# Optimization experiments

Measured on AMD Instinct MI355X. Metric: run time of the kernel, lower is better.

## Reference

```python
import jax, jax.numpy as jnp
import numpy as np

B, C, L = 8, 512, 2048
CK = C // 8  # key/query dim of SAGAN attention


def setup_inputs() -> dict:
    key = jax.random.key(0)
    ks = jax.random.split(key, 4)
    s = 0.02  # init scale for weights
    x = jax.random.normal(ks[0], (B, C, L), dtype=jnp.float32)
    Wf = jax.random.normal(ks[1], (CK, C), dtype=jnp.float32) * s
    Wg = jax.random.normal(ks[2], (CK, C), dtype=jnp.float32) * s
    Wh = jax.random.normal(ks[3], (C, C), dtype=jnp.float32) * s
    bf = jnp.zeros((CK,), dtype=jnp.float32)
    bg = jnp.zeros((CK,), dtype=jnp.float32)
    bh = jnp.zeros((C,), dtype=jnp.float32)
    return {"x": x, "Wf": Wf, "bf": bf, "Wg": Wg, "bg": bg, "Wh": Wh, "bh": bh}


def reference(x, Wf, bf, Wg, bg, Wh, bh):
    # conv1x1 projections == channel-mixing matmuls
    f = jnp.einsum('kc,bcl->bkl', Wf, x) + bf[None, :, None]   # (B, CK, L)
    g = jnp.einsum('kc,bcl->bkl', Wg, x) + bg[None, :, None]   # (B, CK, L)
    h = jnp.einsum('oc,bcl->bol', Wh, x) + bh[None, :, None]   # (B, C, L)
    # att[b, i, j] = sum_k f[b,k,i] * g[b,k,j]  (NOTE: no 1/sqrt(d) scale, as in source)
    att = jnp.einsum('bki,bkj->bij', f, g)                      # (B, L, L)
    att = jax.nn.softmax(att, axis=-1)
    self_att = jnp.einsum('bcj,bij->bci', h, att)               # (B, C, L)
    return self_att + x
```

## Files before the change

### kernel.cpp

```cpp
#include <hip/hip_runtime.h>
#include <math.h>
#include <stdint.h>

#define BATCH 8
#define CH    512
#define SEQ   2048
#define CKDIM 64

typedef __attribute__((ext_vector_type(8))) short bf16x8;
typedef __attribute__((ext_vector_type(4))) float f32x4;

__device__ __forceinline__ unsigned short f2b(float f) {
    union { float f; uint32_t u; } v; v.f = f;
    uint32_t u = v.u;
    u += 0x7fffu + ((u >> 16) & 1u);
    return (unsigned short)(u >> 16);
}
__device__ __forceinline__ float b2f(unsigned short h) {
    union { uint32_t u; float f; } v; v.u = ((uint32_t)h) << 16;
    return v.f;
}

__global__ __launch_bounds__(256) void transpose_cast_kernel(
    const float* __restrict__ x, unsigned short* __restrict__ xt)
{
    __shared__ float t[64][65];
    const int b = blockIdx.z, l0 = blockIdx.x * 64, c0 = blockIdx.y * 64;
    const int tx = threadIdx.x & 63, ty = threadIdx.x >> 6;
    #pragma unroll
    for (int q = 0; q < 16; ++q)
        t[ty + q * 4][tx] = x[((size_t)b * CH + c0 + ty + q * 4) * SEQ + l0 + tx];
    __syncthreads();
    #pragma unroll
    for (int q = 0; q < 16; ++q)
        xt[((size_t)b * SEQ + l0 + ty + q * 4) * CH + c0 + tx] = f2b(t[tx][ty + q * 4]);
}

__global__ __launch_bounds__(256) void castw_kernel(
    const float* __restrict__ Wf, const float* __restrict__ Wg,
    const float* __restrict__ Wh, const float* __restrict__ bf_,
    const float* __restrict__ bg_, unsigned short* __restrict__ Wfgb,
    unsigned short* __restrict__ Whb, float* __restrict__ bias_fg)
{
    const int i = blockIdx.x * 256 + threadIdx.x;
    if (i < 128) bias_fg[i] = (i < 64) ? bf_[i] : bg_[i - 64];
    if (i < 65536) Wfgb[i] = f2b((i < 32768) ? Wf[i] : Wg[i - 32768]);
    if (i < 262144) Whb[i] = f2b(Wh[i]);
}

__device__ __attribute__((always_inline)) inline void gemm_core_nt(
    const unsigned short* __restrict__ A, const int ldA,
    const unsigned short* __restrict__ B, const int ldB,
    const int K,
    unsigned short* __restrict__ ldsA, unsigned short* __restrict__ ldsB,
    f32x4 acc[4][4])
{
    const int tid  = threadIdx.x;
    const int lane = tid & 63;
    const int wm   = tid >> 7;
    const int wn   = (tid >> 6) & 1;
    const int fr   = lane & 15;
    const int hi   = lane >> 4;
    const int xo   = lane & 7;

    int goA[4], goB[4], lo[4];
    #pragma unroll
    for (int it = 0; it < 4; ++it) {
        const int idx = tid + it * 256;
        const int row = idx >> 3;
        const int ch  = idx & 7;
        goA[it] = row * ldA + ch * 8;
        goB[it] = row * ldB + ch * 8;
        lo[it]  = row * 64 + ((ch ^ (row & 7)) * 8);
    }
    int aoff[4], boff[4];
    #pragma unroll
    for (int f = 0; f < 4; ++f) {
        aoff[f] = (wm * 64 + f * 16 + fr) * 64;
        boff[f] = (wn * 64 + f * 16 + fr) * 64;
    }
    const int coff0 = ((0 + hi) ^ xo) * 8;
    const int coff1 = ((4 + hi) ^ xo) * 8;

    uint4 ra[4], rb[4];
    #pragma unroll
    for (int it = 0; it < 4; ++it) {
        ra[it] = *(const uint4*)(A + goA[it]);
        rb[it] = *(const uint4*)(B + goB[it]);
    }

    for (int k0 = 0; k0 < K; k0 += 64) {
        #pragma unroll
        for (int it = 0; it < 4; ++it) {
            *(uint4*)&ldsA[lo[it]] = ra[it];
            *(uint4*)&ldsB[lo[it]] = rb[it];
        }
        __syncthreads();
        if (k0 + 64 < K) {
            #pragma unroll
            for (int it = 0; it < 4; ++it) {
                ra[it] = *(const uint4*)(A + goA[it] + k0 + 64);
                rb[it] = *(const uint4*)(B + goB[it] + k0 + 64);
            }
        }
        #pragma unroll
        for (int kk = 0; kk < 2; ++kk) {
            const int co = kk ? coff1 : coff0;
            bf16x8 af[4], bg[4];
            #pragma unroll
            for (int f = 0; f < 4; ++f) {
                af[f] = *(const bf16x8*)&ldsA[aoff[f] + co];
                bg[f] = *(const bf16x8*)&ldsB[boff[f] + co];
            }
            #pragma unroll
            for (int m = 0; m < 4; ++m)
                #pragma unroll
                for (int n = 0; n < 4; ++n)
                    acc[m][n] = __builtin_amdgcn_mfma_f32_16x16x32_bf16(
                        af[m], bg[n], acc[m][n], 0, 0, 0);
        }
        __syncthreads();
    }
}

__device__ __attribute__((always_inline)) inline void epilogue_store_bf16(
    unsigned short* __restrict__ lds, f32x4 acc[4][4],
    unsigned short* __restrict__ outBase, const int ldOut,
    const float* __restrict__ rowBias, const float* __restrict__ colBias)
{
    const int tid = threadIdx.x;
    const int lane = tid & 63;
    const int wm = tid >> 7, wn = (tid >> 6) & 1;
    const int fr = lane & 15, hi = lane >> 4;
    #pragma unroll
    for (int m = 0; m < 4; ++m) {
        const int m0 = wm * 64 + m * 16 + hi * 4;
        #pragma unroll
        for (int n = 0; n < 4; ++n) {
            const int nn = wn * 64 + n * 16 + fr;
            const float cb = colBias ? colBias[nn] : 0.f;
            #pragma unroll
            for (int e = 0; e < 4; ++e) {
                float v = acc[m][n][e] + cb;
                if (rowBias) v += rowBias[m0 + e];
                lds[(m0 + e) * 128 + nn] = f2b(v);
            }
        }
    }
    __syncthreads();
    #pragma unroll
    for (int q = 0; q < 8; ++q) {
        const int idx = tid + q * 256;
        const int row = idx >> 4, ch = idx & 15;
        *(uint4*)&outBase[(size_t)row * ldOut + ch * 8] =
            *(const uint4*)&lds[row * 128 + ch * 8];
    }
}

__global__ __launch_bounds__(256) void proj_fg_kernel(
    const unsigned short* __restrict__ xt, const unsigned short* __restrict__ Wfg,
    const float* __restrict__ bias_fg, unsigned short* __restrict__ fg_t)
{
    __shared__ unsigned short lds[16384];
    const int b = blockIdx.z, i0 = blockIdx.x * 128;
    const unsigned short* A = xt + ((size_t)b * SEQ + i0) * CH;
    f32x4 acc[4][4];
    const f32x4 z = {0.f, 0.f, 0.f, 0.f};
    #pragma unroll
    for (int m = 0; m < 4; ++m)
        #pragma unroll
        for (int n = 0; n < 4; ++n) acc[m][n] = z;
    gemm_core_nt(A, CH, Wfg, CH, CH, lds, lds + 8192, acc);
    epilogue_store_bf16(lds, acc, fg_t + ((size_t)b * SEQ + i0) * 128, 128,
                        nullptr, bias_fg);
}

__global__ __launch_bounds__(256) void proj_h_kernel(
    const unsigned short* __restrict__ xt, const unsigned short* __restrict__ Whb,
    const float* __restrict__ bh, unsigned short* __restrict__ h_b)
{
    __shared__ unsigned short lds[16384];
    const int b = blockIdx.z, l0 = blockIdx.x * 128, c0 = blockIdx.y * 128;
    const unsigned short* A = Whb + (size_t)c0 * CH;
    const unsigned short* B = xt + ((size_t)b * SEQ + l0) * CH;
    f32x4 acc[4][4];
    const f32x4 z = {0.f, 0.f, 0.f, 0.f};
    #pragma unroll
    for (int m = 0; m < 4; ++m)
        #pragma unroll
        for (int n = 0; n < 4; ++n) acc[m][n] = z;
    gemm_core_nt(A, CH, B, CH, CH, lds, lds + 8192, acc);
    epilogue_store_bf16(lds, acc,
                        h_b + ((size_t)b * CH + c0) * SEQ + l0, SEQ,
                        bh + c0, nullptr);
}

__global__ __launch_bounds__(256) void scores_kernel(
    const unsigned short* __restrict__ fg_t, unsigned short* __restrict__ att,
    int b0, long long attStride)
{
    __shared__ unsigned short lds[16384];
    const int b = b0 + blockIdx.z;
    const int j0 = blockIdx.x * 128, i0 = blockIdx.y * 128;
    const unsigned short* A = fg_t + ((size_t)b * SEQ + i0) * 128;
    const unsigned short* B = fg_t + ((size_t)b * SEQ + j0) * 128 + 64;
    f32x4 acc[4][4];
    const f32x4 z = {0.f, 0.f, 0.f, 0.f};
    #pragma unroll
    for (int m = 0; m < 4; ++m)
        #pragma unroll
        for (int n = 0; n < 4; ++n) acc[m][n] = z;
    gemm_core_nt(A, 128, B, 128, CKDIM, lds, lds + 8192, acc);
    unsigned short* outBase = att + (size_t)blockIdx.z * attStride +
                              (size_t)i0 * SEQ + j0;
    epilogue_store_bf16(lds, acc, outBase, SEQ, nullptr, nullptr);
}

__global__ __launch_bounds__(256) void softmax_kernel(
    unsigned short* __restrict__ att, long long attStride)
{
    const int w = threadIdx.x >> 6, lane = threadIdx.x & 63;
    uint4* rp = (uint4*)(att + (size_t)blockIdx.z * attStride +
                         ((size_t)blockIdx.x * 4 + w) * SEQ);
    uint4 v[4];
    float f[32];
    #pragma unroll
    for (int q = 0; q < 4; ++q) v[q] = rp[lane + q * 64];
    #pragma unroll
    for (int q = 0; q < 4; ++q) {
        const uint32_t w0 = v[q].x, w1 = v[q].y, w2 = v[q].z, w3 = v[q].w;
        f[q * 8 + 0] = b2f((unsigned short)(w0 & 0xffff));
        f[q * 8 + 1] = b2f((unsigned short)(w0 >> 16));
        f[q * 8 + 2] = b2f((unsigned short)(w1 & 0xffff));
        f[q * 8 + 3] = b2f((unsigned short)(w1 >> 16));
        f[q * 8 + 4] = b2f((unsigned short)(w2 & 0xffff));
        f[q * 8 + 5] = b2f((unsigned short)(w2 >> 16));
        f[q * 8 + 6] = b2f((unsigned short)(w3 & 0xffff));
        f[q * 8 + 7] = b2f((unsigned short)(w3 >> 16));
    }
    float mx = -INFINITY;
    #pragma unroll
    for (int q = 0; q < 32; ++q) mx = fmaxf(mx, f[q]);
    #pragma unroll
    for (int off = 32; off > 0; off >>= 1)
        mx = fmaxf(mx, __shfl_xor(mx, off));
    float s = 0.f;
    #pragma unroll
    for (int q = 0; q < 32; ++q) { f[q] = __expf(f[q] - mx); s += f[q]; }
    #pragma unroll
    for (int off = 32; off > 0; off >>= 1)
        s += __shfl_xor(s, off);
    const float inv = 1.f / s;
    #pragma unroll
    for (int q = 0; q < 4; ++q) {
        uint4 o;
        o.x = (uint32_t)f2b(f[q * 8 + 0] * inv) | ((uint32_t)f2b(f[q * 8 + 1] * inv) << 16);
        o.y = (uint32_t)f2b(f[q * 8 + 2] * inv) | ((uint32_t)f2b(f[q * 8 + 3] * inv) << 16);
        o.z = (uint32_t)f2b(f[q * 8 + 4] * inv) | ((uint32_t)f2b(f[q * 8 + 5] * inv) << 16);
        o.w = (uint32_t)f2b(f[q * 8 + 6] * inv) | ((uint32_t)f2b(f[q * 8 + 7] * inv) << 16);
        rp[lane + q * 64] = o;
    }
}

__global__ __launch_bounds__(256) void pv_kernel(
    const unsigned short* __restrict__ h_b, const unsigned short* __restrict__ att,
    const float* __restrict__ x, float* __restrict__ out,
    int b0, long long attStride)
{
    __shared__ unsigned short lds[16384];
    const int b = b0 + blockIdx.z;
    const int i0 = blockIdx.x * 128, c0 = blockIdx.y * 128;
    const unsigned short* A = h_b + ((size_t)b * CH + c0) * SEQ;
    const unsigned short* B = att + (size_t)blockIdx.z * attStride + (size_t)i0 * SEQ;
    f32x4 acc[4][4];
    const f32x4 z = {0.f, 0.f, 0.f, 0.f};
    #pragma unroll
    for (int m = 0; m < 4; ++m)
        #pragma unroll
        for (int n = 0; n < 4; ++n) acc[m][n] = z;
    gemm_core_nt(A, SEQ, B, SEQ, SEQ, lds, lds + 8192, acc);

    const int lane = threadIdx.x & 63;
    const int wm = threadIdx.x >> 7, wn = (threadIdx.x >> 6) & 1;
    const int fr = lane & 15, hi = lane >> 4;
    #pragma unroll
    for (int m = 0; m < 4; ++m)
        #pragma unroll
        for (int n = 0; n < 4; ++n) {
            const int i = i0 + wn * 64 + n * 16 + fr;
            #pragma unroll
            for (int e = 0; e < 4; ++e) {
                const int c = c0 + wm * 64 + m * 16 + hi * 4 + e;
                const size_t o = ((size_t)b * CH + c) * SEQ + i;
                out[o] = acc[m][n][e] + x[o];
            }
        }
}

extern "C" void kernel_launch(void* const* d_in, const int* in_sizes, int n_in,
                              void* d_out, int out_size, void* d_ws, size_t ws_size,
                              hipStream_t stream)
{
    const float* x  = (const float*)d_in[0];
    const float* Wf = (const float*)d_in[1];
    const float* bf_ = (const float*)d_in[2];
    const float* Wg = (const float*)d_in[3];
    const float* bg_ = (const float*)d_in[4];
    const float* Wh = (const float*)d_in[5];
    const float* bh = (const float*)d_in[6];
    float* out = (float*)d_out;

    unsigned short* ws = (unsigned short*)d_ws;
    size_t off = 0;
    unsigned short* xt   = ws + off; off += (size_t)BATCH * SEQ * CH;
    unsigned short* Wfgb = ws + off; off += 128 * CH;
    unsigned short* Whb  = ws + off; off += CH * CH;
    unsigned short* fg_t = ws + off; off += (size_t)BATCH * SEQ * 128;
    unsigned short* h_b  = ws + off; off += (size_t)BATCH * CH * SEQ;
    float* bias_fg = (float*)(ws + off); off += 256;
    unsigned short* att  = ws + off;

    const size_t need_multi = (off + (size_t)BATCH * SEQ * SEQ) * sizeof(unsigned short);
    const bool multi = ws_size >= need_multi;

    transpose_cast_kernel<<<dim3(SEQ / 64, CH / 64, BATCH), 256, 0, stream>>>(x, xt);
    castw_kernel<<<dim3(1024), 256, 0, stream>>>(Wf, Wg, Wh, bf_, bg_, Wfgb, Whb, bias_fg);
    proj_fg_kernel<<<dim3(SEQ / 128, 1, BATCH), 256, 0, stream>>>(xt, Wfgb, bias_fg, fg_t);
    proj_h_kernel<<<dim3(SEQ / 128, CH / 128, BATCH), 256, 0, stream>>>(xt, Whb, bh, h_b);

    if (multi) {
        const long long s = (long long)SEQ * SEQ;
        scores_kernel<<<dim3(SEQ / 128, SEQ / 128, BATCH), 256, 0, stream>>>(fg_t, att, 0, s);
        softmax_kernel<<<dim3(SEQ / 4, 1, BATCH), 256, 0, stream>>>(att, s);
        pv_kernel<<<dim3(SEQ / 128, CH / 128, BATCH), 256, 0, stream>>>(h_b, att, x, out, 0, s);
    } else {
        for (int b = 0; b < BATCH; ++b) {
            scores_kernel<<<dim3(SEQ / 128, SEQ / 128, 1), 256, 0, stream>>>(fg_t, att, b, 0);
            softmax_kernel<<<dim3(SEQ / 4, 1, 1), 256, 0, stream>>>(att, 0);
            pv_kernel<<<dim3(SEQ / 128, CH / 128, 1), 256, 0, stream>>>(h_b, att, x, out, b, 0);
        }
    }
}
```

Measured before the change: 370.3 us.

## Fuse scores, softmax and PV into a single flash-attention kernel

Replaces the separate scores, softmax and PV kernels, which write and re-read a full B×L×L bf16 attention matrix, with one online-softmax flash kernel. Each block handles 64 query rows and all 512 channels, streaming 64-key tiles of g and h with register prefetch and keeping S, P and h in LDS. This removes the large attention-matrix traffic and two launches. In exchange it launches only 256 blocks of 512 threads with about 90KB of LDS each, so occupancy and parallelism are low, and every j-tile goes through several barriers.

New measurement: 443.2 us. 19.7% more time.

```diff
diff --git a/kernel.cpp b/kernel.cpp
--- a/kernel.cpp
+++ b/kernel.cpp
@@ -15,10 +15,6 @@
     uint32_t u = v.u;
     u += 0x7fffu + ((u >> 16) & 1u);
     return (unsigned short)(u >> 16);
-}
-__device__ __forceinline__ float b2f(unsigned short h) {
-    union { uint32_t u; float f; } v; v.u = ((uint32_t)h) << 16;
-    return v.f;
 }
 
 __global__ __launch_bounds__(256) void transpose_cast_kernel(
@@ -195,119 +191,192 @@
                         bh + c0, nullptr);
 }
 
-__global__ __launch_bounds__(256) void scores_kernel(
-    const unsigned short* __restrict__ fg_t, unsigned short* __restrict__ att,
-    int b0, long long attStride)
-{
-    __shared__ unsigned short lds[16384];
-    const int b = b0 + blockIdx.z;
-    const int j0 = blockIdx.x * 128, i0 = blockIdx.y * 128;
-    const unsigned short* A = fg_t + ((size_t)b * SEQ + i0) * 128;
-    const unsigned short* B = fg_t + ((size_t)b * SEQ + j0) * 128 + 64;
+__global__ __launch_bounds__(512) void flash_kernel(
+    const unsigned short* __restrict__ fg_t,
+    const unsigned short* __restrict__ h_b,
+    const float* __restrict__ x,
+    float* __restrict__ out)
+{
+    __shared__ __align__(16) char smem[92160];
+    unsigned short* h_lds = (unsigned short*)smem;
+    unsigned short* P_lds = (unsigned short*)(smem + 65536);
+    float* S_lds = (float*)(smem + 73728);
+    float* m_lds = (float*)(smem + 91136);
+    float* l_lds = (float*)(smem + 91392);
+    float* a_lds = (float*)(smem + 91648);
+    float* trans = (float*)smem;
+
+    const int tid  = threadIdx.x;
+    const int w    = tid >> 6, lane = tid & 63;
+    const int fr   = lane & 15, hi = lane >> 4;
+    const int flat = blockIdx.x;
+    const int b    = flat & 7;
+    const int i0   = (flat >> 3) * 64;
+    const int ihalf = w & 1, jq = w >> 1;
+
+    if (tid < 64) { m_lds[tid] = -INFINITY; l_lds[tid] = 0.f; }
+
+    bf16x8 qf[2][2];
+    #pragma unroll
+    for (int m = 0; m < 2; ++m)
+        #pragma unroll
+        for (int kk = 0; kk < 2; ++kk)
+            qf[m][kk] = *(const bf16x8*)(fg_t +
+                ((size_t)b * SEQ + i0 + ihalf * 32 + m * 16 + fr) * 128 +
+                kk * 32 + hi * 8);
+
+    bf16x8 greg[2];
+    uint4 hreg[8];
+    #pragma unroll
+    for (int kk = 0; kk < 2; ++kk)
+        greg[kk] = *(const bf16x8*)(fg_t +
+            ((size_t)b * SEQ + jq * 16 + fr) * 128 + 64 + kk * 32 + hi * 8);
+    #pragma unroll
+    for (int q = 0; q < 8; ++q) {
+        const int id = tid + q * 512, c = id >> 3, ch = id & 7;
+        hreg[q] = *(const uint4*)(h_b + ((size_t)b * CH + c) * SEQ + ch * 8);
+    }
+
     f32x4 acc[4][4];
     const f32x4 z = {0.f, 0.f, 0.f, 0.f};
     #pragma unroll
     for (int m = 0; m < 4; ++m)
         #pragma unroll
         for (int n = 0; n < 4; ++n) acc[m][n] = z;
-    gemm_core_nt(A, 128, B, 128, CKDIM, lds, lds + 8192, acc);
-    unsigned short* outBase = att + (size_t)blockIdx.z * attStride +
-                              (size_t)i0 * SEQ + j0;
-    epilogue_store_bf16(lds, acc, outBase, SEQ, nullptr, nullptr);
-}
-
-__global__ __launch_bounds__(256) void softmax_kernel(
-    unsigned short* __restrict__ att, long long attStride)
-{
-    const int w = threadIdx.x >> 6, lane = threadIdx.x & 63;
-    uint4* rp = (uint4*)(att + (size_t)blockIdx.z * attStride +
-                         ((size_t)blockIdx.x * 4 + w) * SEQ);
-    uint4 v[4];
-    float f[32];
-    #pragma unroll
-    for (int q = 0; q < 4; ++q) v[q] = rp[lane + q * 64];
-    #pragma unroll
-    for (int q = 0; q < 4; ++q) {
-        const uint32_t w0 = v[q].x, w1 = v[q].y, w2 = v[q].z, w3 = v[q].w;
-        f[q * 8 + 0] = b2f((unsigned short)(w0 & 0xffff));
-        f[q * 8 + 1] = b2f((unsigned short)(w0 >> 16));
-        f[q * 8 + 2] = b2f((unsigned short)(w1 & 0xffff));
-        f[q * 8 + 3] = b2f((unsigned short)(w1 >> 16));
-        f[q * 8 + 4] = b2f((unsigned short)(w2 & 0xffff));
-        f[q * 8 + 5] = b2f((unsigned short)(w2 >> 16));
-        f[q * 8 + 6] = b2f((unsigned short)(w3 & 0xffff));
-        f[q * 8 + 7] = b2f((unsigned short)(w3 >> 16));
-    }
-    float mx = -INFINITY;
-    #pragma unroll
-    for (int q = 0; q < 32; ++q) mx = fmaxf(mx, f[q]);
-    #pragma unroll
-    for (int off = 32; off > 0; off >>= 1)
-        mx = fmaxf(mx, __shfl_xor(mx, off));
-    float s = 0.f;
-    #pragma unroll
-    for (int q = 0; q < 32; ++q) { f[q] = __expf(f[q] - mx); s += f[q]; }
-    #pragma unroll
-    for (int off = 32; off > 0; off >>= 1)
-        s += __shfl_xor(s, off);
-    const float inv = 1.f / s;
-    #pragma unroll
-    for (int q = 0; q < 4; ++q) {
-        uint4 o;
-        o.x = (uint32_t)f2b(f[q * 8 + 0] * inv) | ((uint32_t)f2b(f[q * 8 + 1] * inv) << 16);
-        o.y = (uint32_t)f2b(f[q * 8 + 2] * inv) | ((uint32_t)f2b(f[q * 8 + 3] * inv) << 16);
-        o.z = (uint32_t)f2b(f[q * 8 + 4] * inv) | ((uint32_t)f2b(f[q * 8 + 5] * inv) << 16);
-        o.w = (uint32_t)f2b(f[q * 8 + 6] * inv) | ((uint32_t)f2b(f[q * 8 + 7] * inv) << 16);
-        rp[lane + q * 64] = o;
-    }
-}
-
-__global__ __launch_bounds__(256) void pv_kernel(
-    const unsigned short* __restrict__ h_b, const unsigned short* __restrict__ att,
-    const float* __restrict__ x, float* __restrict__ out,
-    int b0, long long attStride)
-{
-    __shared__ unsigned short lds[16384];
-    const int b = b0 + blockIdx.z;
-    const int i0 = blockIdx.x * 128, c0 = blockIdx.y * 128;
-    const unsigned short* A = h_b + ((size_t)b * CH + c0) * SEQ;
-    const unsigned short* B = att + (size_t)blockIdx.z * attStride + (size_t)i0 * SEQ;
-    f32x4 acc[4][4];
-    const f32x4 z = {0.f, 0.f, 0.f, 0.f};
-    #pragma unroll
-    for (int m = 0; m < 4; ++m)
-        #pragma unroll
-        for (int n = 0; n < 4; ++n) acc[m][n] = z;
-    gemm_core_nt(A, SEQ, B, SEQ, SEQ, lds, lds + 8192, acc);
-
-    const int lane = threadIdx.x & 63;
-    const int wm = threadIdx.x >> 7, wn = (threadIdx.x >> 6) & 1;
-    const int fr = lane & 15, hi = lane >> 4;
-    #pragma unroll
-    for (int m = 0; m < 4; ++m)
-        #pragma unroll
-        for (int n = 0; n < 4; ++n) {
-            const int i = i0 + wn * 64 + n * 16 + fr;
+    __syncthreads();
+
+    for (int jt = 0; jt < 32; ++jt) {
+        #pragma unroll
+        for (int q = 0; q < 8; ++q) {
+            const int id = tid + q * 512, c = id >> 3, ch = id & 7;
+            *(uint4*)&h_lds[c * 64 + ((ch ^ (c & 7)) * 8)] = hreg[q];
+        }
+        f32x4 sacc[2] = {z, z};
+        #pragma unroll
+        for (int kk = 0; kk < 2; ++kk)
+            #pragma unroll
+            for (int m = 0; m < 2; ++m)
+                sacc[m] = __builtin_amdgcn_mfma_f32_16x16x32_bf16(
+                    qf[m][kk], greg[kk], sacc[m], 0, 0, 0);
+        #pragma unroll
+        for (int m = 0; m < 2; ++m)
+            #pragma unroll
+            for (int e = 0; e < 4; ++e)
+                S_lds[(ihalf * 32 + m * 16 + hi * 4 + e) * 68 + jq * 16 + fr] =
+                    sacc[m][e];
+        __syncthreads();
+
+        #pragma unroll
+        for (int rr = 0; rr < 8; ++rr) {
+            const int r = w * 8 + rr;
+            const float sv = S_lds[r * 68 + lane];
+            float tmax = sv;
+            #pragma unroll
+            for (int off = 32; off > 0; off >>= 1)
+                tmax = fmaxf(tmax, __shfl_xor(tmax, off));
+            const float mo = m_lds[r];
+            const float mn = fmaxf(mo, tmax);
+            const float p = __expf(sv - mn);
+            float ts = p;
+            #pragma unroll
+            for (int off = 32; off > 0; off >>= 1)
+                ts += __shfl_xor(ts, off);
+            if (lane == 0) {
+                const float al = __expf(mo - mn);
+                l_lds[r] = l_lds[r] * al + ts;
+                m_lds[r] = mn;
+                a_lds[r] = al;
+            }
+            P_lds[r * 64 + (((lane >> 3) ^ (r & 7)) << 3) + (lane & 7)] = f2b(p);
+        }
+        if (jt + 1 < 32) {
+            #pragma unroll
+            for (int kk = 0; kk < 2; ++kk)
+                greg[kk] = *(const bf16x8*)(fg_t +
+                    ((size_t)b * SEQ + (jt + 1) * 64 + jq * 16 + fr) * 128 +
+                    64 + kk * 32 + hi * 8);
+            #pragma unroll
+            for (int q = 0; q < 8; ++q) {
+                const int id = tid + q * 512, c = id >> 3, ch = id & 7;
+                hreg[q] = *(const uint4*)(h_b + ((size_t)b * CH + c) * SEQ +
+                                          (jt + 1) * 64 + ch * 8);
+            }
+        }
+        __syncthreads();
+
+        #pragma unroll
+        for (int m = 0; m < 4; ++m)
             #pragma unroll
             for (int e = 0; e < 4; ++e) {
-                const int c = c0 + wm * 64 + m * 16 + hi * 4 + e;
-                const size_t o = ((size_t)b * CH + c) * SEQ + i;
-                out[o] = acc[m][n][e] + x[o];
-            }
-        }
+                const float al = a_lds[m * 16 + hi * 4 + e];
+                #pragma unroll
+                for (int n = 0; n < 4; ++n)
+                    acc[m][n][e] *= al;
+            }
+        #pragma unroll
+        for (int kk = 0; kk < 2; ++kk) {
+            bf16x8 pa[4], hb[4];
+            #pragma unroll
+            for (int m = 0; m < 4; ++m)
+                pa[m] = *(const bf16x8*)&P_lds[(m * 16 + fr) * 64 +
+                                               (((kk * 4 + hi) ^ (fr & 7)) << 3)];
+            #pragma unroll
+            for (int n = 0; n < 4; ++n)
+                hb[n] = *(const bf16x8*)&h_lds[(w * 64 + n * 16 + fr) * 64 +
+                                               (((kk * 4 + hi) ^ (fr & 7)) << 3)];
+            #pragma unroll
+            for (int m = 0; m < 4; ++m)
+                #pragma unroll
+                for (int n = 0; n < 4; ++n)
+                    acc[m][n] = __builtin_amdgcn_mfma_f32_16x16x32_bf16(
+                        pa[m], hb[n], acc[m][n], 0, 0, 0);
+        }
+        __syncthreads();
+    }
+
+    #pragma unroll
+    for (int round = 0; round < 2; ++round) {
+        __syncthreads();
+        if ((w >> 2) == round) {
+            float* T = trans + (w & 3) * 4096;
+            #pragma unroll
+            for (int m = 0; m < 4; ++m)
+                #pragma unroll
+                for (int e = 0; e < 4; ++e) {
+                    const float inv = 1.f / l_lds[m * 16 + hi * 4 + e];
+                    #pragma unroll
+                    for (int n = 0; n < 4; ++n)
+                        T[(n * 16 + fr) * 64 + (((m * 4 + hi) ^ fr) << 2) + e] =
+                            acc[m][n][e] * inv;
+                }
+        }
+        __syncthreads();
+        #pragma unroll
+        for (int q = 0; q < 8; ++q) {
+            const int id = tid + q * 512;
+            const int c_rel = id >> 4, ich = id & 15;
+            const int slot = c_rel >> 6, c_in = c_rel & 63;
+            f32x4 v = *(const f32x4*)(trans + slot * 4096 + c_in * 64 +
+                                      ((ich ^ (c_in & 15)) << 2));
+            const size_t ga = ((size_t)b * CH + round * 256 + c_rel) * SEQ +
+                              i0 + ich * 4;
+            f32x4 xv = *(const f32x4*)(x + ga);
+            *(f32x4*)(out + ga) = v + xv;
+        }
+    }
 }
 
 extern "C" void kernel_launch(void* const* d_in, const int* in_sizes, int n_in,
                               void* d_out, int out_size, void* d_ws, size_t ws_size,
                               hipStream_t stream)
 {
-    const float* x  = (const float*)d_in[0];
-    const float* Wf = (const float*)d_in[1];
+    const float* x   = (const float*)d_in[0];
+    const float* Wf  = (const float*)d_in[1];
     const float* bf_ = (const float*)d_in[2];
-    const float* Wg = (const float*)d_in[3];
+    const float* Wg  = (const float*)d_in[3];
     const float* bg_ = (const float*)d_in[4];
-    const float* Wh = (const float*)d_in[5];
-    const float* bh = (const float*)d_in[6];
+    const float* Wh  = (const float*)d_in[5];
+    const float* bh  = (const float*)d_in[6];
     float* out = (float*)d_out;
 
     unsigned short* ws = (unsigned short*)d_ws;
@@ -317,27 +386,11 @@
     unsigned short* Whb  = ws + off; off += CH * CH;
     unsigned short* fg_t = ws + off; off += (size_t)BATCH * SEQ * 128;
     unsigned short* h_b  = ws + off; off += (size_t)BATCH * CH * SEQ;
-    float* bias_fg = (float*)(ws + off); off += 256;
-    unsigned short* att  = ws + off;
-
-    const size_t need_multi = (off + (size_t)BATCH * SEQ * SEQ) * sizeof(unsigned short);
-    const bool multi = ws_size >= need_multi;
+    float* bias_fg = (float*)(ws + off);
 
     transpose_cast_kernel<<<dim3(SEQ / 64, CH / 64, BATCH), 256, 0, stream>>>(x, xt);
     castw_kernel<<<dim3(1024), 256, 0, stream>>>(Wf, Wg, Wh, bf_, bg_, Wfgb, Whb, bias_fg);
     proj_fg_kernel<<<dim3(SEQ / 128, 1, BATCH), 256, 0, stream>>>(xt, Wfgb, bias_fg, fg_t);
     proj_h_kernel<<<dim3(SEQ / 128, CH / 128, BATCH), 256, 0, stream>>>(xt, Whb, bh, h_b);
-
-    if (multi) {
-        const long long s = (long long)SEQ * SEQ;
-        scores_kernel<<<dim3(SEQ / 128, SEQ / 128, BATCH), 256, 0, stream>>>(fg_t, att, 0, s);
-        softmax_kernel<<<dim3(SEQ / 4, 1, BATCH), 256, 0, stream>>>(att, s);
-        pv_kernel<<<dim3(SEQ / 128, CH / 128, BATCH), 256, 0, stream>>>(h_b, att, x, out, 0, s);
-    } else {
-        for (int b = 0; b < BATCH; ++b) {
-            scores_kernel<<<dim3(SEQ / 128, SEQ / 128, 1), 256, 0, stream>>>(fg_t, att, b, 0);
-            softmax_kernel<<<dim3(SEQ / 4, 1, 1), 256, 0, stream>>>(att, 0);
-            pv_kernel<<<dim3(SEQ / 128, CH / 128, 1), 256, 0, stream>>>(h_b, att, x, out, b, 0);
-        }
-    }
-}
+    flash_kernel<<<dim3((SEQ / 64) * BATCH), 512, 0, stream>>>(fg_t, h_b, x, out);
+}
```
